# Optimization experiments

Measured on AMD Instinct MI355X. Metric: run time of the kernel, lower is better.

Reference implementation:

```python
import jax, jax.numpy as jnp
import numpy as np

B, N, DIM, H, D = 1, 1024, 512, 8, 64
BC, BS, K, W = 16, 16, 8, 256   # compress blk, selection blk, top-k blocks, sliding window
C = N // BC                     # number of compression / selection blocks
SCALE = D ** -0.5
EPS = 1e-6
NEG = -1e30


def rmsnorm(x):
    return x * jax.lax.rsqrt(jnp.mean(x * x, axis=-1, keepdims=True) + EPS)


def rope(x):  # x: [B,H,N,D], GPT-NeoX style half rotation
    half = D // 2
    inv = 1.0 / (10000.0 ** (jnp.arange(half, dtype=jnp.float32) / half))
    ang = jnp.arange(x.shape[2], dtype=jnp.float32)[:, None] * inv
    cos, sin = jnp.cos(ang), jnp.sin(ang)
    x1, x2 = x[..., :half], x[..., half:]
    return jnp.concatenate([x1 * cos - x2 * sin, x2 * cos + x1 * sin], axis=-1).astype(x.dtype)


def setup_inputs():
    key = jax.random.key(0)
    ks = jax.random.split(key, 24)
    w = lambda k, shape, fan: jax.random.normal(k, shape, jnp.float32) * (fan ** -0.5)
    return {
        'x':  jax.random.normal(ks[0], (B, N, DIM), jnp.float32),
        've': jax.random.normal(ks[1], (B, N, DIM), jnp.float32),
        'x0': jax.random.normal(ks[2], (B, N, DIM), jnp.float32),
        'lambdas': jnp.array([1.0, 0.0], jnp.float32),
        'Wq': w(ks[3], (DIM, H * D), DIM),
        'Wk': w(ks[4], (DIM, H * D), DIM),
        'Wv': w(ks[5], (DIM, H * D), DIM),
        'Wo': w(ks[6], (H * D, DIM), H * D),
        'Wg': w(ks[7], (DIM, 3 * H), DIM),
        'k_pos': w(ks[8], (H, BC, D), D),
        'v_pos': w(ks[9], (H, BC, D), D),
        'Wck': w(ks[10], (BC * D, D), BC * D),
        'bck': jnp.zeros((D,), jnp.float32),
        'Wcv': w(ks[11], (BC * D, D), BC * D),
        'bcv': jnp.zeros((D,), jnp.float32),
        'k_mem': w(ks[12], (H, 1, D), D),
        'v_mem': w(ks[13], (H, 1, D), D),
        'W1': w(ks[14], (DIM, 4 * DIM), DIM),
        'W2': w(ks[15], (4 * DIM, DIM), 4 * DIM),
    }


def _nsa_attn(xn, Wq, Wk, Wv, Wo, Wg, k_pos, v_pos, Wck, bck, Wcv, bcv, k_mem, v_mem):
    q = (xn @ Wq).reshape(B, N, H, D).transpose(0, 2, 1, 3)   # [B,H,N,D]
    k = (xn @ Wk).reshape(B, N, H, D).transpose(0, 2, 1, 3)
    v = (xn @ Wv).reshape(B, N, H, D).transpose(0, 2, 1, 3)
    q, k = rope(q), rope(k)
    i_idx = jnp.arange(N)

    # ---- compressed branch: pool kv into blocks via learned linear + intra-block pos emb ----
    kb = k.reshape(B, H, C, BC, D) + k_pos[None, :, None]
    vb = v.reshape(B, H, C, BC, D) + v_pos[None, :, None]
    ck = kb.reshape(B, H, C, BC * D) @ Wck + bck              # [B,H,C,D]
    cv = vb.reshape(B, H, C, BC * D) @ Wcv + bcv
    ckf = jnp.concatenate([jnp.broadcast_to(k_mem[None], (B, H, 1, D)), ck], axis=2)
    cvf = jnp.concatenate([jnp.broadcast_to(v_mem[None], (B, H, 1, D)), cv], axis=2)
    csim = jnp.einsum('bhid,bhjd->bhij', q, ckf) * SCALE      # [B,H,N,C+1]
    past = ((jnp.arange(C) + 1) * BC - 1)[None, :] < i_idx[:, None]   # block fully in the past
    cmask = jnp.concatenate([jnp.ones((N, 1), bool), past], axis=1)   # mem kv always visible
    cattn = jax.nn.softmax(jnp.where(cmask[None, None], csim, NEG), axis=-1)
    c_out = jnp.einsum('bhij,bhjd->bhid', cattn, cvf)

    # ---- fine selection branch: top-K blocks by compressed attention importance ----
    imp = jnp.where(past[None, None], cattn[..., 1:], NEG)    # [B,H,N,C]
    vals, sel = jax.lax.top_k(imp, K)                         # [B,H,N,K]
    valid = vals >= 0.0                                       # drop picks among masked blocks
    kb_f = k.reshape(B, H, C, BS, D)
    vb_f = v.reshape(B, H, C, BS, D)
    k_sel = jnp.take_along_axis(kb_f[:, :, None], sel[..., None, None], axis=3)  # [B,H,N,K,BS,D]
    v_sel = jnp.take_along_axis(vb_f[:, :, None], sel[..., None, None], axis=3)
    own = i_idx // BS                                         # query's own block, causal inside
    k_fine = jnp.concatenate([k_sel, kb_f[:, :, own][:, :, :, None]], axis=3)    # [B,H,N,K+1,BS,D]
    v_fine = jnp.concatenate([v_sel, vb_f[:, :, own][:, :, :, None]], axis=3)
    offs = jnp.arange(BS)
    m_sel = (sel[..., None] * BS + offs <= i_idx[None, None, :, None, None]) & valid[..., None]
    m_own = jnp.broadcast_to((own[:, None] * BS + offs <= i_idx[:, None])[None, None, :, None], (B, H, N, 1, BS))
    m_fine = jnp.concatenate([m_sel, m_own], axis=3)
    fsim = jnp.where(m_fine, jnp.einsum('bhnd,bhnksd->bhnks', q, k_fine) * SCALE, NEG)
    fattn = jax.nn.softmax(fsim.reshape(B, H, N, (K + 1) * BS), axis=-1).reshape(B, H, N, K + 1, BS)
    f_out = jnp.einsum('bhnks,bhnksd->bhnd', fattn, v_fine)

    # ---- sliding window branch ----
    smask = (i_idx[None, :] <= i_idx[:, None]) & (i_idx[:, None] - i_idx[None, :] < W)
    ssim = jnp.where(smask[None, None], jnp.einsum('bhid,bhjd->bhij', q, k) * SCALE, NEG)
    s_out = jnp.einsum('bhij,bhjd->bhid', jax.nn.softmax(ssim, axis=-1), v)

    # ---- per-head sigmoid gates combine the three strategies ----
    gates = jax.nn.sigmoid(xn @ Wg).reshape(B, N, H, 3).transpose(0, 2, 1, 3)  # [B,H,N,3]
    o = gates[..., 0:1] * c_out + gates[..., 1:2] * f_out + gates[..., 2:3] * s_out
    return o.transpose(0, 2, 1, 3).reshape(B, N, H * D) @ Wo


def reference(x, ve, x0, lambdas, Wq, Wk, Wv, Wo, Wg, k_pos, v_pos, Wck, bck, Wcv, bcv, k_mem, v_mem, W1, W2):
    # ve is accepted by NSABlock.forward but never consumed in this block
    x = lambdas[0] * x + lambdas[1] * x0
    x = x + _nsa_attn(rmsnorm(x), Wq, Wk, Wv, Wo, Wg, k_pos, v_pos, Wck, bck, Wcv, bcv, k_mem, v_mem)
    x = x + jnp.square(jax.nn.relu(rmsnorm(x) @ W1)) @ W2
    return x
```

## Files before the change

### kernel.cpp

```cpp
#include <hip/hip_runtime.h>
#include <math.h>

#define NTOK 1024
#define DIMM 512
#define NH 8
#define HD 64
#define BCB 16
#define BSB 16
#define KSEL 8
#define WWIN 256
#define CBLK 64
#define SCALE 0.125f
#define EPSV 1e-6f
#define NEGV -1e30f

typedef short bf16x8 __attribute__((ext_vector_type(8)));
typedef float f32x4 __attribute__((ext_vector_type(4)));

__device__ inline ushort f2b(float f) {
  union { float f; unsigned int u; } c; c.f = f;
  unsigned int u = c.u;
  return (ushort)((u + 0x7FFFu + ((u >> 16) & 1u)) >> 16);
}
__device__ inline float b2f(ushort h) {
// ... 201 lines not shown
  const int Kd = 2048;
  __shared__ ushort As[64 * 40];
  __shared__ ushort Bs[64 * 40];
  int tid = threadIdx.x;
  int lane = tid & 63, w = tid >> 6;
  int rb = blockIdx.y * 64, cb = blockIdx.x * 64;
  int kb = blockIdx.z * 1024;
  int wm = (w >> 1) * 32, wn = (w & 1) * 32;
  int quad = lane >> 4, l15 = lane & 15;
  int srow = tid >> 2, scol = (tid & 3) * 8;

  f32x4 acc[2][2];
#pragma unroll
  for (int i = 0; i < 2; i++)
#pragma unroll
    for (int j = 0; j < 2; j++) acc[i][j] = (f32x4){0.f, 0.f, 0.f, 0.f};

  const ushort* ap = A  + (size_t)(rb + srow) * Kd + kb + scol;
  const ushort* bp = BT + (size_t)(cb + srow) * Kd + kb + scol;
  ushort* aw = &As[srow * 40 + scol];
  ushort* bw = &Bs[srow * 40 + scol];

  int4 pa = *(const int4*)ap;
  int4 pb = *(const int4*)bp;

  for (int k0 = 0; k0 < 1024; k0 += 32) {
    if (k0) __syncthreads();
    *(int4*)aw = pa;
    *(int4*)bw = pb;
    __syncthreads();
    if (k0 + 32 < 1024) {
      pa = *(const int4*)(ap + k0 + 32);
      pb = *(const int4*)(bp + k0 + 32);
    }
    bf16x8 af[2], bfr[2];
#pragma unroll
    for (int t = 0; t < 2; t++) {
      af[t]  = *(const bf16x8*)&As[(wm + t * 16 + l15) * 40 + quad * 8];
      bfr[t] = *(const bf16x8*)&Bs[(wn + t * 16 + l15) * 40 + quad * 8];
    }
#pragma unroll
    for (int i = 0; i < 2; i++)
#pragma unroll
      for (int j = 0; j < 2; j++)
        acc[i][j] = __builtin_amdgcn_mfma_f32_16x16x32_bf16(af[i], bfr[j],
                                                            acc[i][j], 0, 0, 0);
  }

#pragma unroll
  for (int i = 0; i < 2; i++) {
#pragma unroll
    for (int j = 0; j < 2; j++) {
      int col = cb + wn + j * 16 + l15;
#pragma unroll
      for (int r = 0; r < 4; r++) {
        int row = rb + wm + i * 16 + quad * 4 + r;
        atomicAdd(&outb[(size_t)row * 512 + col], acc[i][j][r]);
      }
    }
  }
}

__global__ void __launch_bounds__(256)
k_gemm_wo(const float* __restrict__ cg, const float* __restrict__ fg,
          const float* __restrict__ sg, const float* __restrict__ gates,
          const ushort* __restrict__ BT, float* __restrict__ P0,
          float* __restrict__ P1) {
  __shared__ ushort As[64 * 40];
  __shared__ ushort Bs[64 * 40];
  int tid = threadIdx.x;
  int lane = tid & 63, wave = tid >> 6;
  int rb = blockIdx.y * 64, cb = blockIdx.x * 64;
  int kb = blockIdx.z * 256;
  int wm = (wave >> 1) * 32, wn = (wave & 1) * 32;
  int q = lane >> 4, l15 = lane & 15;
  int srow = tid >> 2, scol = (tid & 3) * 8;

  f32x4 acc[2][2];
#pragma unroll
  for (int i = 0; i < 2; i++)
#pragma unroll
    for (int j = 0; j < 2; j++) acc[i][j] = (f32x4){0.f, 0.f, 0.f, 0.f};

  int row = rb + srow;
  const ushort* bp = BT + (size_t)(cb + srow) * 512 + kb + scol;
  ushort* aw = &As[srow * 40 + scol];
  ushort* bw = &Bs[srow * 40 + scol];

  for (int k0 = 0; k0 < 256; k0 += 32) {
    int colb = kb + k0 + scol;
    int hh = colb >> 6;
    const float* gp = gates + (size_t)row * 24 + hh * 3;
    float g0 = gp[0], g1 = gp[1], g2 = gp[2];
    size_t off = (size_t)row * 512 + colb;
    float4 c0 = *(const float4*)(cg + off), c1 = *(const float4*)(cg + off + 4);
    float4 f0 = *(const float4*)(fg + off), f1 = *(const float4*)(fg + off + 4);
    float4 s0 = *(const float4*)(sg + off), s1 = *(const float4*)(sg + off + 4);
    float va[8] = {g0 * c0.x + g1 * f0.x + g2 * s0.x,
                   g0 * c0.y + g1 * f0.y + g2 * s0.y,
                   g0 * c0.z + g1 * f0.z + g2 * s0.z,
                   g0 * c0.w + g1 * f0.w + g2 * s0.w,
                   g0 * c1.x + g1 * f1.x + g2 * s1.x,
                   g0 * c1.y + g1 * f1.y + g2 * s1.y,
                   g0 * c1.z + g1 * f1.z + g2 * s1.z,
                   g0 * c1.w + g1 * f1.w + g2 * s1.w};
    ushort h[8];
#pragma unroll
    for (int e = 0; e < 8; e++) h[e] = f2b(va[e]);
    *(int4*)aw = *(int4*)h;
    *(int4*)bw = *(const int4*)(bp + k0);
    __syncthreads();
    bf16x8 af[2], bfr[2];
#pragma unroll
    for (int t = 0; t < 2; t++) {
      af[t]  = *(const bf16x8*)&As[(wm + t * 16 + l15) * 40 + q * 8];
      bfr[t] = *(const bf16x8*)&Bs[(wn + t * 16 + l15) * 40 + q * 8];
    }
#pragma unroll
    for (int i = 0; i < 2; i++)
#pragma unroll
      for (int j = 0; j < 2; j++)
        acc[i][j] = __builtin_amdgcn_mfma_f32_16x16x32_bf16(af[i], bfr[j],
                                                            acc[i][j], 0, 0, 0);
    __syncthreads();
  }

  float* pbuf = blockIdx.z ? P1 : P0;
#pragma unroll
  for (int i = 0; i < 2; i++) {
#pragma unroll
    for (int j = 0; j < 2; j++) {
      int col = cb + wn + j * 16 + l15;
#pragma unroll
      for (int r = 0; r < 4; r++) {
        int rr = rb + wm + i * 16 + q * 4 + r;
        pbuf[(size_t)rr * 512 + col] = acc[i][j][r];
      }
    }
  }
}

__global__ void __launch_bounds__(256)
k_gemm_qkv(const ushort* __restrict__ Ah, const ushort* __restrict__ Al,
           const ushort* __restrict__ BTh, const ushort* __restrict__ BTl,
           float* __restrict__ qout, ushort* __restrict__ khm_h,
           ushort* __restrict__ khm_l, ushort* __restrict__ vhm_h,
           ushort* __restrict__ vhm_l, float* __restrict__ gates,
           const float* __restrict__ ctab, const float* __restrict__ stab) {
  const int Kd = 512;
  __shared__ ushort SM[15360];
  ushort* Ash = SM;
  ushort* Asl = SM + 5120;
  ushort* Bsh = SM + 10240;
  ushort* Bsl = SM + 12800;
  int tid = threadIdx.x;
  int lane = tid & 63, wave = tid >> 6;
  int rb = blockIdx.y * 128, cb = blockIdx.x * 64;
  const bool prec = (cb < 1024);
  int wm = (wave >> 1) * 64, wn = (wave & 1) * 32;
  int q = lane >> 4, l15 = lane & 15;
  int srA = tid >> 1, scA = (tid & 1) * 16;
  int srB = tid >> 2, scB = (tid & 3) * 8;

  f32x4 acc[4][2];
#pragma unroll
  for (int i = 0; i < 4; i++)
#pragma unroll
    for (int j = 0; j < 2; j++) acc[i][j] = (f32x4){0.f, 0.f, 0.f, 0.f};

  const ushort* aph = Ah  + (size_t)(rb + srA) * Kd + scA;
  const ushort* apl = Al  + (size_t)(rb + srA) * Kd + scA;
  const ushort* bph = BTh + (size_t)(cb + srB) * Kd + scB;
  const ushort* bpl = BTl + (size_t)(cb + srB) * Kd + scB;
  ushort* awh = &Ash[srA * 40 + scA];
  ushort* awl = &Asl[srA * 40 + scA];
  ushort* bwh = &Bsh[srB * 40 + scB];
  ushort* bwl = &Bsl[srB * 40 + scB];

  int4 ph0 = *(const int4*)aph;
  int4 ph1 = *(const int4*)(aph + 8);
  int4 pbh = *(const int4*)bph;
  int4 pl0, pl1, pbl;
  if (prec) {
    pl0 = *(const int4*)apl;
    pl1 = *(const int4*)(apl + 8);
    pbl = *(const int4*)bpl;
  }

  for (int k0 = 0; k0 < Kd; k0 += 32) {
    if (k0) __syncthreads();
    *(int4*)awh = ph0; *(int4*)(awh + 8) = ph1;
    *(int4*)bwh = pbh;
    if (prec) {
      *(int4*)awl = pl0; *(int4*)(awl + 8) = pl1;
      *(int4*)bwl = pbl;
    }
    __syncthreads();
    if (k0 + 32 < Kd) {
      ph0 = *(const int4*)(aph + k0 + 32);
      ph1 = *(const int4*)(aph + k0 + 40);
      pbh = *(const int4*)(bph + k0 + 32);
      if (prec) {
        pl0 = *(const int4*)(apl + k0 + 32);
        pl1 = *(const int4*)(apl + k0 + 40);
        pbl = *(const int4*)(bpl + k0 + 32);
      }
    }
    bf16x8 afh[4], bfh[2], afl[4], bfl[2];
#pragma unroll
    for (int t = 0; t < 4; t++)
      afh[t] = *(const bf16x8*)&Ash[(wm + t * 16 + l15) * 40 + q * 8];
#pragma unroll
    for (int t = 0; t < 2; t++)
      bfh[t] = *(const bf16x8*)&Bsh[(wn + t * 16 + l15) * 40 + q * 8];
    if (prec) {
#pragma unroll
      for (int t = 0; t < 4; t++)
        afl[t] = *(const bf16x8*)&Asl[(wm + t * 16 + l15) * 40 + q * 8];
#pragma unroll
      for (int t = 0; t < 2; t++)
        bfl[t] = *(const bf16x8*)&Bsl[(wn + t * 16 + l15) * 40 + q * 8];
    }
#pragma unroll
    for (int i = 0; i < 4; i++)
#pragma unroll
      for (int j = 0; j < 2; j++) {
        acc[i][j] = __builtin_amdgcn_mfma_f32_16x16x32_bf16(afh[i], bfh[j],
                                                            acc[i][j], 0, 0, 0);
        if (prec) {
          acc[i][j] = __builtin_amdgcn_mfma_f32_16x16x32_bf16(afh[i], bfl[j],
                                                              acc[i][j], 0, 0, 0);
          acc[i][j] = __builtin_amdgcn_mfma_f32_16x16x32_bf16(afl[i], bfh[j],
                                                              acc[i][j], 0, 0, 0);
        }
      }
  }

  if (prec) {
    float* st = (float*)SM;
    int h = (cb & 511) >> 6;
#pragma unroll
    for (int hb = 0; hb < 2; hb++) {
      __syncthreads();
      if ((wave >> 1) == hb) {
#pragma unroll
        for (int i = 0; i < 4; i++)
#pragma unroll
          for (int j = 0; j < 2; j++)
#pragma unroll
            for (int r = 0; r < 4; r++)
              st[(i * 16 + q * 4 + r) * 66 + wn + j * 16 + l15] = acc[i][j][r];
      }
      __syncthreads();
#pragma unroll
      for (int e = 0; e < 8; e++) {
        int p = e * 256 + tid;
        int rw = p >> 5, d = p & 31;
        int n = rb + hb * 64 + rw;
        float x1 = st[rw * 66 + d], x2 = st[rw * 66 + d + 32];
        float cs = ctab[n * 32 + d], sn = stab[n * 32 + d];
        float o1 = x1 * cs - x2 * sn;
        float o2 = x2 * cs + x1 * sn;
        if (cb < 512) {
          qout[(size_t)n * 512 + h * 64 + d]      = o1;
          qout[(size_t)n * 512 + h * 64 + d + 32] = o2;
        } else {
          size_t ob = (size_t)h * 65536 + (size_t)n * 64 + d;
          ushort b1 = f2b(o1), b2v = f2b(o2);
          khm_h[ob]      = b1;
          khm_h[ob + 32] = b2v;
          khm_l[ob]      = f2b(o1 - b2f(b1));
          khm_l[ob + 32] = f2b(o2 - b2f(b2v));
        }
      }
    }
  } else {
#pragma unroll
    for (int i = 0; i < 4; i++) {
#pragma unroll
      for (int j = 0; j < 2; j++) {
        int col = cb + wn + j * 16 + l15;
#pragma unroll
        for (int r = 0; r < 4; r++) {
          int row = rb + wm + i * 16 + q * 4 + r;
          float vv = acc[i][j][r];
          if (cb >= 1536) {
            int c24 = col - 1536;
            if (c24 < 24)
              gates[(size_t)row * 24 + c24] = 1.f / (1.f + expf(-vv));
          } else {
            int c = col - 1024;
            size_t ob = (size_t)(c >> 6) * 65536 + (size_t)row * 64 + (c & 63);
            ushort hb = f2b(vv);
            vhm_h[ob] = hb;
            vhm_l[ob] = f2b(vv - b2f(hb));
          }
        }
      }
    }
  }
}

__global__ void __launch_bounds__(256)
k_mid(const ushort* __restrict__ khm_h, const ushort* __restrict__ khm_l,
      const ushort* __restrict__ vhm_h, const ushort* __restrict__ vhm_l,
      const ushort* __restrict__ WckTh, const ushort* __restrict__ WckTl,
      const ushort* __restrict__ WcvTh, const ushort* __restrict__ WcvTl,
      const float* __restrict__ pwk, const float* __restrict__ pwv,
      float* __restrict__ ckb, float* __restrict__ cvb,
      const float* __restrict__ qg, float* __restrict__ sout) {
  __shared__ union {
    struct { ushort Ash[32 * 72]; ushort Asl[32 * 72];
             ushort Bsh[64 * 72]; ushort Bsl[64 * 72]; } c;
    struct { ushort Kt[64 * 72]; ushort VT[64 * 72];
             ushort Qs[64 * 72]; ushort Ps[4][16 * 72]; } s;
  } U;
  int tid = threadIdx.x, lane = tid & 63, w = tid >> 6;
  int quad = lane >> 4, l15 = lane & 15;

  if (blockIdx.x < 32) {
    int h = blockIdx.x & 7, kv = (blockIdx.x >> 3) & 1, mh = blockIdx.x >> 4;
    const ushort* sH = kv ? vhm_h : khm_h;
    const ushort* sL = kv ? vhm_l : khm_l;
    const ushort* WTh = kv ? WcvTh : WckTh;
    const ushort* WTl = kv ? WcvTl : WckTl;
    const float* pw = (kv ? pwv : pwk) + h * 64;
    float* outp = kv ? cvb : ckb;

    ushort* Ash = U.c.Ash; ushort* Asl = U.c.Asl;
    ushort* Bsh = U.c.Bsh; ushort* Bsl = U.c.Bsl;
    int wmi = w >> 1, wnj = w & 1;
    int arow = tid >> 3, ae0 = (tid & 7) * 8;
    int brow = tid >> 2, be0 = (tid & 3) * 16;
    size_t abase = (size_t)h * 65536 + (size_t)(mh * 32 + arow) * 1024 + ae0;
    size_t bbase = (size_t)brow * 1024 + be0;

    f32x4 acc[2];
#pragma unroll
    for (int j = 0; j < 2; j++) acc[j] = (f32x4){0.f, 0.f, 0.f, 0.f};

    for (int t = 0; t < 16; t++) {
      int kb = t * 64;
      *(int4*)&Ash[arow * 72 + ae0] = *(const int4*)(sH + abase + kb);
      *(int4*)&Asl[arow * 72 + ae0] = *(const int4*)(sL + abase + kb);
      *(int4*)&Bsh[brow * 72 + be0]     = *(const int4*)(WTh + bbase + kb);
      *(int4*)&Bsh[brow * 72 + be0 + 8] = *(const int4*)(WTh + bbase + kb + 8);
      *(int4*)&Bsl[brow * 72 + be0]     = *(const int4*)(WTl + bbase + kb);
      *(int4*)&Bsl[brow * 72 + be0 + 8] = *(const int4*)(WTl + bbase + kb + 8);
      __syncthreads();
#pragma unroll
      for (int sub = 0; sub < 2; sub++) {
        int ar2 = (wmi * 16 + l15) * 72 + sub * 32 + quad * 8;
        bf16x8 afh = *(const bf16x8*)&Ash[ar2];
        bf16x8 afl = *(const bf16x8*)&Asl[ar2];
#pragma unroll
        for (int j = 0; j < 2; j++) {
          int br2 = (wnj * 32 + j * 16 + l15) * 72 + sub * 32 + quad * 8;
          bf16x8 bfh = *(const bf16x8*)&Bsh[br2];
          bf16x8 bfl = *(const bf16x8*)&Bsl[br2];
          acc[j] = __builtin_amdgcn_mfma_f32_16x16x32_bf16(afh, bfh, acc[j], 0, 0, 0);
          acc[j] = __builtin_amdgcn_mfma_f32_16x16x32_bf16(afh, bfl, acc[j], 0, 0, 0);
          acc[j] = __builtin_amdgcn_mfma_f32_16x16x32_bf16(afl, bfh, acc[j], 0, 0, 0);
        }
      }
      __syncthreads();
    }

#pragma unroll
    for (int j = 0; j < 2; j++) {
      int d = wnj * 32 + j * 16 + l15;
      float bv = pw[d];
#pragma unroll
      for (int r = 0; r < 4; r++) {
        int c = mh * 32 + wmi * 16 + quad * 4 + r;
        outp[((size_t)h * 64 + c) * 64 + d] = acc[j][r] + bv;
      }
    }
  } else {
    int sidx = blockIdx.x - 32;
    int h = sidx >> 4, i0 = (sidx & 15) * 64;
    ushort* Kt = U.s.Kt; ushort* VT = U.s.VT; ushort* Qs = U.s.Qs;

#pragma unroll
    for (int it = 0; it < 2; it++) {
      int f = it * 256 + tid;
      int r = f >> 3, d0 = (f & 7) * 8;
      const float* qp = qg + (size_t)(i0 + r) * DIMM + h * HD + d0;
      float4 t0 = *(const float4*)qp;
      float4 t1 = *(const float4*)(qp + 4);
      ushort u[8] = {f2b(t0.x), f2b(t0.y), f2b(t0.z), f2b(t0.w),
                     f2b(t1.x), f2b(t1.y), f2b(t1.z), f2b(t1.w)};
      *(int4*)&Qs[r * 72 + d0] = *(int4*)u;
    }

    int lo = i0 - (WWIN - 1); if (lo < 0) lo = 0;
    int jb_lo = lo >> 6, jb_hi = (i0 + 63) >> 6;

    float mrow[4], lrow[4];
    f32x4 Of[4];
#pragma unroll
    for (int r = 0; r < 4; r++) { mrow[r] = NEGV; lrow[r] = 0.f; }
#pragma unroll
    for (int d = 0; d < 4; d++) Of[d] = (f32x4){0.f, 0.f, 0.f, 0.f};

    for (int jb = jb_lo; jb <= jb_hi; jb++) {
      __syncthreads();
#pragma unroll
      for (int it = 0; it < 2; it++) {
        int f = it * 256 + tid;
        int r = f >> 3, c8 = (f & 7) * 8;
        const ushort* kp = khm_h + (size_t)h * 65536 + (size_t)(jb * 64 + r) * 64 + c8;
        *(int4*)&Kt[r * 72 + c8] = *(const int4*)kp;
        const ushort* vp = vhm_h + (size_t)h * 65536 + (size_t)(jb * 64 + r) * 64 + c8;
        ushort vv[8];
        *(int4*)vv = *(const int4*)vp;
#pragma unroll
        for (int e = 0; e < 8; e++) VT[(c8 + e) * 72 + r] = vv[e];
      }
      __syncthreads();

      bf16x8 qa[2];
#pragma unroll
      for (int c = 0; c < 2; c++)
        qa[c] = *(const bf16x8*)&Qs[(w * 16 + l15) * 72 + c * 32 + quad * 8];

      f32x4 sc[4];
      __builtin_amdgcn_s_setprio(1);
#pragma unroll
      for (int ks = 0; ks < 4; ks++) {
        f32x4 a = (f32x4){0.f, 0.f, 0.f, 0.f};
#pragma unroll
        for (int c = 0; c < 2; c++) {
          bf16x8 kb = *(const bf16x8*)&Kt[(ks * 16 + l15) * 72 + c * 32 + quad * 8];
          a = __builtin_amdgcn_mfma_f32_16x16x32_bf16(qa[c], kb, a, 0, 0, 0);
        }
        sc[ks] = a;
      }
      __builtin_amdgcn_s_setprio(0);

      float pm[4][4], rmax[4];
#pragma unroll
      for (int r = 0; r < 4; r++) rmax[r] = NEGV;
#pragma unroll
      for (int ks = 0; ks < 4; ks++) {
        int gj = jb * 64 + ks * 16 + l15;
#pragma unroll
        for (int r = 0; r < 4; r++) {
          int qi = i0 + w * 16 + quad * 4 + r;
          bool vis = (gj <= qi) && (qi - gj < WWIN);
          float s = vis ? sc[ks][r] * SCALE : NEGV;
          pm[ks][r] = s;
          rmax[r] = fmaxf(rmax[r], s);
        }
      }
#pragma unroll
      for (int off = 1; off < 16; off <<= 1)
#pragma unroll
        for (int r = 0; r < 4; r++)
          rmax[r] = fmaxf(rmax[r], __shfl_xor(rmax[r], off));

      float alpha[4], rsum[4];
#pragma unroll
      for (int r = 0; r < 4; r++) {
        float newm = fmaxf(mrow[r], rmax[r]);
        alpha[r] = expf(mrow[r] - newm);
        mrow[r] = newm;
        rsum[r] = 0.f;
      }
#pragma unroll
      for (int ks = 0; ks < 4; ks++)
#pragma unroll
        for (int r = 0; r < 4; r++) {
          float p = expf(pm[ks][r] - mrow[r]);
          pm[ks][r] = p;
          rsum[r] += p;
        }
#pragma unroll
      for (int off = 1; off < 16; off <<= 1)
#pragma unroll
        for (int r = 0; r < 4; r++)
          rsum[r] += __shfl_xor(rsum[r], off);
#pragma unroll
      for (int r = 0; r < 4; r++)
        lrow[r] = lrow[r] * alpha[r] + rsum[r];

#pragma unroll
      for (int ks = 0; ks < 4; ks++)
#pragma unroll
        for (int r = 0; r < 4; r++)
          U.s.Ps[w][(quad * 4 + r) * 72 + ks * 16 + l15] = f2b(pm[ks][r]);
#pragma unroll
      for (int d = 0; d < 4; d++)
#pragma unroll
        for (int r = 0; r < 4; r++)
          Of[d][r] *= alpha[r];

      __builtin_amdgcn_s_setprio(1);
#pragma unroll
      for (int c = 0; c < 2; c++) {
        bf16x8 pa = *(const bf16x8*)&U.s.Ps[w][l15 * 72 + c * 32 + quad * 8];
#pragma unroll
        for (int d = 0; d < 4; d++) {
          bf16x8 vb = *(const bf16x8*)&VT[(d * 16 + l15) * 72 + c * 32 + quad * 8];
          Of[d] = __builtin_amdgcn_mfma_f32_16x16x32_bf16(pa, vb, Of[d], 0, 0, 0);
        }
      }
      __builtin_amdgcn_s_setprio(0);
    }

#pragma unroll
    for (int d = 0; d < 4; d++)
#pragma unroll
      for (int r = 0; r < 4; r++) {
        int qi = i0 + w * 16 + quad * 4 + r;
        sout[(size_t)qi * DIMM + h * HD + d * 16 + l15] = Of[d][r] / lrow[r];
      }
  }
}

__global__ void __launch_bounds__(256)
k_cmpf(const float* __restrict__ qg, const float* __restrict__ ckb,
       const float* __restrict__ cvb, const float* __restrict__ k_mem,
       const float* __restrict__ v_mem, const ushort* __restrict__ khm_h,
       const ushort* __restrict__ vhm_h, float* __restrict__ cout,
       float* __restrict__ fout) {
  int h = blockIdx.y, i0 = blockIdx.x * 4;
  int tid = threadIdx.x, lane = tid & 63, w = tid >> 6;
  __shared__ float ckt[64][65];
  __shared__ float cvs[64][65];
  __shared__ float qs[4][64];
  __shared__ float kms[64], vms[64];
  __shared__ float sp[4][64];
  __shared__ float spf[4][144];

#pragma unroll
  for (int r = 0; r < 4; r++) {
    int f = r * 256 + tid;
    int c = f >> 4, d0 = (f & 15) * 4;
    float4 t = *(const float4*)(ckb + ((size_t)h * 64 + c) * 64 + d0);
    ckt[d0][c] = t.x; ckt[d0 + 1][c] = t.y; ckt[d0 + 2][c] = t.z; ckt[d0 + 3][c] = t.w;
    float4 u = *(const float4*)(cvb + ((size_t)h * 64 + c) * 64 + d0);
    cvs[c][d0] = u.x; cvs[c][d0 + 1] = u.y; cvs[c][d0 + 2] = u.z; cvs[c][d0 + 3] = u.w;
  }
  if (tid < 64) {
    int r = tid >> 4, d0 = (tid & 15) * 4;
    float4 t = *(const float4*)(qg + (size_t)(i0 + r) * DIMM + h * HD + d0);
    qs[r][d0] = t.x; qs[r][d0 + 1] = t.y; qs[r][d0 + 2] = t.z; qs[r][d0 + 3] = t.w;
  } else if (tid < 128) {
    kms[tid - 64] = k_mem[h * HD + tid - 64];
  } else if (tid < 192) {
    vms[tid - 128] = v_mem[h * HD + tid - 128];
  }
  __syncthreads();

  const ushort* kbase = khm_h + (size_t)h * 65536;
  const ushort* vbase = vhm_h + (size_t)h * 65536;

  int qi = i0 + w;
  {
    float dot = 0.f, dm = 0.f;
#pragma unroll 8
    for (int e = 0; e < 64; e++) {
      float qe = qs[w][e];
      dot = fmaf(qe, ckt[e][lane], dot);
      dm  = fmaf(qe, kms[e], dm);
    }
    bool vis = (lane * BCB + BCB - 1) < qi;
    float sj = vis ? dot * SCALE : NEGV;
    float smem = dm * SCALE;
    float m = wred_max(fmaxf(sj, smem));
    float p = expf(sj - m);
    float pmem = expf(smem - m);
    float l = wred_sum(p) + pmem;
    float inv = 1.f / l;

    int selreg = -1;
    float impv = vis ? p : NEGV;
#pragma unroll
    for (int kk = 0; kk < KSEL; kk++) {
      float bv = impv; int bi = lane;
#pragma unroll
      for (int off = 32; off > 0; off >>= 1) {
        float ov = __shfl_xor(bv, off);
        int   oi = __shfl_xor(bi, off);
        if (ov > bv || (ov == bv && oi < bi)) { bv = ov; bi = oi; }
      }
      if (lane == kk) selreg = (bv >= 0.f) ? bi : -1;
      if (lane == bi) impv = NEGV;
    }

    sp[w][lane] = p;
    float od = pmem * vms[lane];
#pragma unroll 8
    for (int j = 0; j < 64; j++) od = fmaf(sp[w][j], cvs[j][lane], od);
    cout[(size_t)qi * DIMM + h * HD + lane] = od * inv;

    int own = qi >> 4;
    float slv[3];
#pragma unroll
    for (int t = 0; t < 3; t++) {
      int key = t * 64 + lane;
      float sv = NEGV;
      if (key < 144) {
        int kk = key >> 4, krow = key & 15;
        int bidx; bool fvis;
        if (kk < KSEL) {
          bidx = __shfl(selreg, kk);
          fvis = (bidx >= 0);
          if (!fvis) bidx = 0;
        } else {
          bidx = own;
          fvis = (krow <= (qi & 15));
        }
        const ushort* kr = kbase + (size_t)(bidx * BSB + krow) * 64;
        float fd = 0.f;
#pragma unroll
        for (int e8 = 0; e8 < 8; e8++) {
          ushort kv8[8];
          *(int4*)kv8 = *(const int4*)(kr + e8 * 8);
#pragma unroll
          for (int e = 0; e < 8; e++)
            fd = fmaf(qs[w][e8 * 8 + e], b2f(kv8[e]), fd);
        }
        sv = fvis ? fd * SCALE : NEGV;
      }
      slv[t] = sv;
    }
    float fm = wred_max(fmaxf(fmaxf(slv[0], slv[1]), slv[2]));
    float fsum = 0.f;
#pragma unroll
    for (int t = 0; t < 3; t++) {
      int key = t * 64 + lane;
      if (key < 144) {
        float pv = expf(slv[t] - fm);
        spf[w][key] = pv;
        fsum += pv;
      }
    }
    fsum = wred_sum(fsum);
    float finv = 1.f / fsum;

    float facc = 0.f;
#pragma unroll
    for (int kk = 0; kk < KSEL + 1; kk++) {
      int bidx = (kk < KSEL) ? __shfl(selreg, kk) : own;
      if (bidx < 0) bidx = 0;
      const ushort* vr = vbase + (size_t)(bidx * BSB) * 64 + lane;
#pragma unroll 8
      for (int krow = 0; krow < 16; krow++)
        facc = fmaf(spf[w][kk * 16 + krow], b2f(vr[(size_t)krow * 64]), facc);
    }
    fout[(size_t)qi * DIMM + h * HD + lane] = facc * finv;
  }
}

extern "C" void kernel_launch(void* const* d_in, const int* in_sizes, int n_in,
                              void* d_out, int out_size, void* d_ws, size_t ws_size,
                              hipStream_t stream) {
  const float* x     = (const float*)d_in[0];
  const float* ve    = (const float*)d_in[1]; (void)ve;
  const float* x0    = (const float*)d_in[2];
  const float* lam   = (const float*)d_in[3];
  const float* Wq    = (const float*)d_in[4];
  const float* Wk    = (const float*)d_in[5];
  const float* Wv    = (const float*)d_in[6];
  const float* Wo    = (const float*)d_in[7];
  const float* Wg    = (const float*)d_in[8];
  const float* k_pos = (const float*)d_in[9];
  const float* v_pos = (const float*)d_in[10];
  const float* Wck   = (const float*)d_in[11];
  const float* bck   = (const float*)d_in[12];
  const float* Wcv   = (const float*)d_in[13];
  const float* bcv   = (const float*)d_in[14];
  const float* k_mem = (const float*)d_in[15];
  const float* v_mem = (const float*)d_in[16];
  const float* W1    = (const float*)d_in[17];
  const float* W2    = (const float*)d_in[18];
  float* out = (float*)d_out;
  float* ws  = (float*)d_ws;

  const size_t NW = (size_t)NTOK * DIMM;
  float* xr    = ws;
  float* xn    = ws + 1 * NW;
  float* q     = ws + 2 * NW;
  float* kslot = ws + 3 * NW;
  float* vslot = ws + 4 * NW;
  float* coutb = ws + 5 * NW;
  float* foutb = ws + 6 * NW;
  float* soutb = ws + 7 * NW;
  float* gates = ws + 9 * NW;
  float* ckb   = gates + 32768;
  float* cvb   = ckb + 32768;
  ushort* qkvTh = (ushort*)(cvb + 32768 + 65536);
  ushort* qkvTl = qkvTh + 1600 * 512;
  ushort* WoT   = qkvTl + 1600 * 512;
  ushort* W1T   = WoT   + 512 * 512;
  ushort* W2T   = W1T   + 2048 * 512;
  ushort* WckTh = W2T   + 512 * 2048;
  ushort* WckTl = WckTh + 64 * 1024;
  ushort* WcvTh = WckTl + 64 * 1024;
  ushort* WcvTl = WcvTh + 64 * 1024;
  float* ctab   = (float*)(WcvTl + 64 * 1024);
  float* stab   = ctab + 32768;
  float* pwk    = stab + 32768;
  float* pwv    = pwk + 512;

  ushort* xnh = (ushort*)xn;
  ushort* xnl = xnh + NW;
  ushort* khm_h = (ushort*)kslot;
  ushort* khm_l = khm_h + 524288;
  ushort* vhm_h = (ushort*)vslot;
  ushort* vhm_l = vhm_h + 524288;
  float* p0w = kslot;
  float* p1w = q;
  ushort* ybf = (ushort*)soutb;
  ushort* h1b = (ushort*)q;

  WtrPack pk;
  pk.d[0] = {Wq, qkvTh,              qkvTl,              512, 512,  512};
  pk.d[1] = {Wk, qkvTh + 512 * 512,  qkvTl + 512 * 512,  512, 512,  512};
  pk.d[2] = {Wv, qkvTh + 1024 * 512, qkvTl + 1024 * 512, 512, 512,  512};
  pk.d[3] = {Wo, WoT, nullptr,  512, 512,  512};
  pk.d[4] = {W1, W1T, nullptr,  512, 2048, 2048};
  pk.d[5] = {W2, W2T, nullptr, 2048, 512,  512};
  pk.d[6] = {Wck, WckTh, WckTl, 1024, 64, 64};
  pk.d[7] = {Wcv, WcvTh, WcvTl, 1024, 64, 64};
  pk.d[8] = {Wg, qkvTh + 1536 * 512, qkvTl + 1536 * 512, 512, 24, 64};
  int cum = 0;
  for (int e = 0; e < 9; e++) {
    cum += (pk.d[e].Npad / 32) * (pk.d[e].K / 32);
    pk.cum[e] = cum;
  }

  k_pre<<<cum + NTOK + 128 + 16, 256, 0, stream>>>(
      pk, x, x0, lam, xr, xnh, xnl, ctab, stab,
      k_pos, v_pos, Wck, Wcv, bck, bcv, pwk, pwv);

  k_gemm_qkv<<<dim3(25, NTOK / 128), 256, 0, stream>>>(
      xnh, xnl, qkvTh, qkvTl, q, khm_h, khm_l, vhm_h, vhm_l, gates,
      ctab, stab);

  k_mid<<<160, 256, 0, stream>>>(khm_h, khm_l, vhm_h, vhm_l,
                                 WckTh, WckTl, WcvTh, WcvTl,
                                 pwk, pwv, ckb, cvb, q, soutb);

  k_cmpf<<<dim3(NTOK / 4, NH), 256, 0, stream>>>(
      q, ckb, cvb, k_mem, v_mem, khm_h, vhm_h, coutb, foutb);

  k_gemm_wo<<<dim3(512 / 64, NTOK / 64, 2), 256, 0, stream>>>(
      coutb, foutb, soutb, gates, WoT, p0w, p1w);
  k_rms_bf<<<NTOK, 256, 0, stream>>>(xr, p0w, p1w, out, ybf);

  k_gemm_w1<<<dim3(2048 / 64, NTOK / 128), 256, 0, stream>>>(ybf, W1T, h1b);
  k_gemm_w2<<<dim3(512 / 64, NTOK / 64, 2), 256, 0, stream>>>(h1b, W2T, out);
}
```

Before: 240.6 us.

## Regroup mid-stage kernels: split ckcv GEMM, co-launch sliding-window with compressed/fine attention

The former k_mid kernel fused the compression GEMM (32 blocks) with the sliding-window attention (128 blocks), and k_cmpf ran afterwards. Now the compression GEMM runs alone in a small kernel, and the sliding-window attention is merged with the compressed/fine attention into one 2176-block launch that shares a shared-memory union. The intent is to overlap the sliding-window work with the compressed/selected branch, which depends on the GEMM output, rather than with the short GEMM. The trade-off is a 32-block launch that leaves most of the GPU idle, and a larger shared-memory union that may lower occupancy for the many small compressed-branch blocks.

```diff
diff --git a/kernel.cpp b/kernel.cpp
--- a/kernel.cpp
+++ b/kernel.cpp
@@ -527,82 +527,91 @@
 }
 
 __global__ void __launch_bounds__(256)
-k_mid(const ushort* __restrict__ khm_h, const ushort* __restrict__ khm_l,
-      const ushort* __restrict__ vhm_h, const ushort* __restrict__ vhm_l,
-      const ushort* __restrict__ WckTh, const ushort* __restrict__ WckTl,
-      const ushort* __restrict__ WcvTh, const ushort* __restrict__ WcvTl,
-      const float* __restrict__ pwk, const float* __restrict__ pwv,
-      float* __restrict__ ckb, float* __restrict__ cvb,
-      const float* __restrict__ qg, float* __restrict__ sout) {
+k_ckcv(const ushort* __restrict__ khm_h, const ushort* __restrict__ khm_l,
+       const ushort* __restrict__ vhm_h, const ushort* __restrict__ vhm_l,
+       const ushort* __restrict__ WckTh, const ushort* __restrict__ WckTl,
+       const ushort* __restrict__ WcvTh, const ushort* __restrict__ WcvTl,
+       const float* __restrict__ pwk, const float* __restrict__ pwv,
+       float* __restrict__ ckb, float* __restrict__ cvb) {
+  __shared__ ushort Ash[32 * 72], Asl[32 * 72];
+  __shared__ ushort Bsh[64 * 72], Bsl[64 * 72];
+  int tid = threadIdx.x, lane = tid & 63, w = tid >> 6;
+  int quad = lane >> 4, l15 = lane & 15;
+  int h = blockIdx.x & 7, kv = (blockIdx.x >> 3) & 1, mh = blockIdx.x >> 4;
+  const ushort* sH = kv ? vhm_h : khm_h;
+  const ushort* sL = kv ? vhm_l : khm_l;
+  const ushort* WTh = kv ? WcvTh : WckTh;
+  const ushort* WTl = kv ? WcvTl : WckTl;
+  const float* pw = (kv ? pwv : pwk) + h * 64;
+  float* outp = kv ? cvb : ckb;
+
+  int wmi = w >> 1, wnj = w & 1;
+  int arow = tid >> 3, ae0 = (tid & 7) * 8;
+  int brow = tid >> 2, be0 = (tid & 3) * 16;
+  size_t abase = (size_t)h * 65536 + (size_t)(mh * 32 + arow) * 1024 + ae0;
+  size_t bbase = (size_t)brow * 1024 + be0;
+
+  f32x4 acc[2];
+#pragma unroll
+  for (int j = 0; j < 2; j++) acc[j] = (f32x4){0.f, 0.f, 0.f, 0.f};
+
+  for (int t = 0; t < 16; t++) {
+    int kb = t * 64;
+    *(int4*)&Ash[arow * 72 + ae0] = *(const int4*)(sH + abase + kb);
+    *(int4*)&Asl[arow * 72 + ae0] = *(const int4*)(sL + abase + kb);
+    *(int4*)&Bsh[brow * 72 + be0]     = *(const int4*)(WTh + bbase + kb);
+    *(int4*)&Bsh[brow * 72 + be0 + 8] = *(const int4*)(WTh + bbase + kb + 8);
+    *(int4*)&Bsl[brow * 72 + be0]     = *(const int4*)(WTl + bbase + kb);
+    *(int4*)&Bsl[brow * 72 + be0 + 8] = *(const int4*)(WTl + bbase + kb + 8);
+    __syncthreads();
+#pragma unroll
+    for (int sub = 0; sub < 2; sub++) {
+      int ar2 = (wmi * 16 + l15) * 72 + sub * 32 + quad * 8;
+      bf16x8 afh = *(const bf16x8*)&Ash[ar2];
+      bf16x8 afl = *(const bf16x8*)&Asl[ar2];
+#pragma unroll
+      for (int j = 0; j < 2; j++) {
+        int br2 = (wnj * 32 + j * 16 + l15) * 72 + sub * 32 + quad * 8;
+        bf16x8 bfh = *(const bf16x8*)&Bsh[br2];
+        bf16x8 bfl = *(const bf16x8*)&Bsl[br2];
+        acc[j] = __builtin_amdgcn_mfma_f32_16x16x32_bf16(afh, bfh, acc[j], 0, 0, 0);
+        acc[j] = __builtin_amdgcn_mfma_f32_16x16x32_bf16(afh, bfl, acc[j], 0, 0, 0);
+        acc[j] = __builtin_amdgcn_mfma_f32_16x16x32_bf16(afl, bfh, acc[j], 0, 0, 0);
+      }
+    }
+    __syncthreads();
+  }
+
+#pragma unroll
+  for (int j = 0; j < 2; j++) {
+    int d = wnj * 32 + j * 16 + l15;
+    float bv = pw[d];
+#pragma unroll
+    for (int r = 0; r < 4; r++) {
+      int c = mh * 32 + wmi * 16 + quad * 4 + r;
+      outp[((size_t)h * 64 + c) * 64 + d] = acc[j][r] + bv;
+    }
+  }
+}
+
+__global__ void __launch_bounds__(256)
+k_scf(const float* __restrict__ qg, const ushort* __restrict__ khm_h,
+      const ushort* __restrict__ vhm_h, float* __restrict__ sout,
+      const float* __restrict__ ckb, const float* __restrict__ cvb,
+      const float* __restrict__ k_mem, const float* __restrict__ v_mem,
+      float* __restrict__ cout, float* __restrict__ fout) {
   __shared__ union {
-    struct { ushort Ash[32 * 72]; ushort Asl[32 * 72];
-             ushort Bsh[64 * 72]; ushort Bsl[64 * 72]; } c;
     struct { ushort Kt[64 * 72]; ushort VT[64 * 72];
              ushort Qs[64 * 72]; ushort Ps[4][16 * 72]; } s;
+    struct { float ckt[64][65]; float cvs[64][65]; float qs[4][64];
+             float kms[64]; float vms[64]; float sp[4][64];
+             float spf[4][144]; } c;
   } U;
   int tid = threadIdx.x, lane = tid & 63, w = tid >> 6;
   int quad = lane >> 4, l15 = lane & 15;
 
-  if (blockIdx.x < 32) {
-    int h = blockIdx.x & 7, kv = (blockIdx.x >> 3) & 1, mh = blockIdx.x >> 4;
-    const ushort* sH = kv ? vhm_h : khm_h;
-    const ushort* sL = kv ? vhm_l : khm_l;
-    const ushort* WTh = kv ? WcvTh : WckTh;
-    const ushort* WTl = kv ? WcvTl : WckTl;
-    const float* pw = (kv ? pwv : pwk) + h * 64;
-    float* outp = kv ? cvb : ckb;
-
-    ushort* Ash = U.c.Ash; ushort* Asl = U.c.Asl;
-    ushort* Bsh = U.c.Bsh; ushort* Bsl = U.c.Bsl;
-    int wmi = w >> 1, wnj = w & 1;
-    int arow = tid >> 3, ae0 = (tid & 7) * 8;
-    int brow = tid >> 2, be0 = (tid & 3) * 16;
-    size_t abase = (size_t)h * 65536 + (size_t)(mh * 32 + arow) * 1024 + ae0;
-    size_t bbase = (size_t)brow * 1024 + be0;
-
-    f32x4 acc[2];
-#pragma unroll
-    for (int j = 0; j < 2; j++) acc[j] = (f32x4){0.f, 0.f, 0.f, 0.f};
-
-    for (int t = 0; t < 16; t++) {
-      int kb = t * 64;
-      *(int4*)&Ash[arow * 72 + ae0] = *(const int4*)(sH + abase + kb);
-      *(int4*)&Asl[arow * 72 + ae0] = *(const int4*)(sL + abase + kb);
-      *(int4*)&Bsh[brow * 72 + be0]     = *(const int4*)(WTh + bbase + kb);
-      *(int4*)&Bsh[brow * 72 + be0 + 8] = *(const int4*)(WTh + bbase + kb + 8);
-      *(int4*)&Bsl[brow * 72 + be0]     = *(const int4*)(WTl + bbase + kb);
-      *(int4*)&Bsl[brow * 72 + be0 + 8] = *(const int4*)(WTl + bbase + kb + 8);
-      __syncthreads();
-#pragma unroll
-      for (int sub = 0; sub < 2; sub++) {
-        int ar2 = (wmi * 16 + l15) * 72 + sub * 32 + quad * 8;
-        bf16x8 afh = *(const bf16x8*)&Ash[ar2];
-        bf16x8 afl = *(const bf16x8*)&Asl[ar2];
-#pragma unroll
-        for (int j = 0; j < 2; j++) {
-          int br2 = (wnj * 32 + j * 16 + l15) * 72 + sub * 32 + quad * 8;
-          bf16x8 bfh = *(const bf16x8*)&Bsh[br2];
-          bf16x8 bfl = *(const bf16x8*)&Bsl[br2];
-          acc[j] = __builtin_amdgcn_mfma_f32_16x16x32_bf16(afh, bfh, acc[j], 0, 0, 0);
-          acc[j] = __builtin_amdgcn_mfma_f32_16x16x32_bf16(afh, bfl, acc[j], 0, 0, 0);
-          acc[j] = __builtin_amdgcn_mfma_f32_16x16x32_bf16(afl, bfh, acc[j], 0, 0, 0);
-        }
-      }
-      __syncthreads();
-    }
-
-#pragma unroll
-    for (int j = 0; j < 2; j++) {
-      int d = wnj * 32 + j * 16 + l15;
-      float bv = pw[d];
-#pragma unroll
-      for (int r = 0; r < 4; r++) {
-        int c = mh * 32 + wmi * 16 + quad * 4 + r;
-        outp[((size_t)h * 64 + c) * 64 + d] = acc[j][r] + bv;
-      }
-    }
-  } else {
-    int sidx = blockIdx.x - 32;
+  if (blockIdx.x < 128) {
+    int sidx = blockIdx.x;
     int h = sidx >> 4, i0 = (sidx & 15) * 64;
     ushort* Kt = U.s.Kt; ushort* VT = U.s.VT; ushort* Qs = U.s.Qs;
 
@@ -726,7 +735,7 @@
         bf16x8 pa = *(const bf16x8*)&U.s.Ps[w][l15 * 72 + c * 32 + quad * 8];
 #pragma unroll
         for (int d = 0; d < 4; d++) {
-          bf16x8 vb = *(const bf16x8*)&VT[(d * 16 + l15) * 72 + c * 32 + quad * 8];
+          bf16x8 vb = *(const bf16x8*)&U.s.VT[(d * 16 + l15) * 72 + c * 32 + quad * 8];
           Of[d] = __builtin_amdgcn_mfma_f32_16x16x32_bf16(pa, vb, Of[d], 0, 0, 0);
         }
       }
@@ -740,142 +749,132 @@
         int qi = i0 + w * 16 + quad * 4 + r;
         sout[(size_t)qi * DIMM + h * HD + d * 16 + l15] = Of[d][r] / lrow[r];
       }
-  }
-}
-
-__global__ void __launch_bounds__(256)
-k_cmpf(const float* __restrict__ qg, const float* __restrict__ ckb,
-       const float* __restrict__ cvb, const float* __restrict__ k_mem,
-       const float* __restrict__ v_mem, const ushort* __restrict__ khm_h,
-       const ushort* __restrict__ vhm_h, float* __restrict__ cout,
-       float* __restrict__ fout) {
-  int h = blockIdx.y, i0 = blockIdx.x * 4;
-  int tid = threadIdx.x, lane = tid & 63, w = tid >> 6;
-  __shared__ float ckt[64][65];
-  __shared__ float cvs[64][65];
-  __shared__ float qs[4][64];
-  __shared__ float kms[64], vms[64];
-  __shared__ float sp[4][64];
-  __shared__ float spf[4][144];
-
-#pragma unroll
-  for (int r = 0; r < 4; r++) {
-    int f = r * 256 + tid;
-    int c = f >> 4, d0 = (f & 15) * 4;
-    float4 t = *(const float4*)(ckb + ((size_t)h * 64 + c) * 64 + d0);
-    ckt[d0][c] = t.x; ckt[d0 + 1][c] = t.y; ckt[d0 + 2][c] = t.z; ckt[d0 + 3][c] = t.w;
-    float4 u = *(const float4*)(cvb + ((size_t)h * 64 + c) * 64 + d0);
-    cvs[c][d0] = u.x; cvs[c][d0 + 1] = u.y; cvs[c][d0 + 2] = u.z; cvs[c][d0 + 3] = u.w;
-  }
-  if (tid < 64) {
-    int r = tid >> 4, d0 = (tid & 15) * 4;
-    float4 t = *(const float4*)(qg + (size_t)(i0 + r) * DIMM + h * HD + d0);
-    qs[r][d0] = t.x; qs[r][d0 + 1] = t.y; qs[r][d0 + 2] = t.z; qs[r][d0 + 3] = t.w;
-  } else if (tid < 128) {
-    kms[tid - 64] = k_mem[h * HD + tid - 64];
-  } else if (tid < 192) {
-    vms[tid - 128] = v_mem[h * HD + tid - 128];
-  }
-  __syncthreads();
-
-  const ushort* kbase = khm_h + (size_t)h * 65536;
-  const ushort* vbase = vhm_h + (size_t)h * 65536;
-
-  int qi = i0 + w;
-  {
-    float dot = 0.f, dm = 0.f;
+  } else {
+    int idx = blockIdx.x - 128;
+    int h = idx >> 8, i0 = (idx & 255) * 4;
+
+#pragma unroll
+    for (int r = 0; r < 4; r++) {
+      int f = r * 256 + tid;
+      int c = f >> 4, d0 = (f & 15) * 4;
+      float4 t = *(const float4*)(ckb + ((size_t)h * 64 + c) * 64 + d0);
+      U.c.ckt[d0][c] = t.x; U.c.ckt[d0 + 1][c] = t.y;
+      U.c.ckt[d0 + 2][c] = t.z; U.c.ckt[d0 + 3][c] = t.w;
+      float4 u = *(const float4*)(cvb + ((size_t)h * 64 + c) * 64 + d0);
+      U.c.cvs[c][d0] = u.x; U.c.cvs[c][d0 + 1] = u.y;
+      U.c.cvs[c][d0 + 2] = u.z; U.c.cvs[c][d0 + 3] = u.w;
+    }
+    if (tid < 64) {
+      int r = tid >> 4, d0 = (tid & 15) * 4;
+      float4 t = *(const float4*)(qg + (size_t)(i0 + r) * DIMM + h * HD + d0);
+      U.c.qs[r][d0] = t.x; U.c.qs[r][d0 + 1] = t.y;
+      U.c.qs[r][d0 + 2] = t.z; U.c.qs[r][d0 + 3] = t.w;
+    } else if (tid < 128) {
+      U.c.kms[tid - 64] = k_mem[h * HD + tid - 64];
+    } else if (tid < 192) {
+      U.c.vms[tid - 128] = v_mem[h * HD + tid - 128];
+    }
+    __syncthreads();
+
+    const ushort* kbase = khm_h + (size_t)h * 65536;
+    const ushort* vbase = vhm_h + (size_t)h * 65536;
+
+    int qi = i0 + w;
+    {
+      float dot = 0.f, dm = 0.f;
 #pragma unroll 8
-    for (int e = 0; e < 64; e++) {
-      float qe = qs[w][e];
-      dot = fmaf(qe, ckt[e][lane], dot);
-      dm  = fmaf(qe, kms[e], dm);
-    }
-    bool vis = (lane * BCB + BCB - 1) < qi;
-    float sj = vis ? dot * SCALE : NEGV;
-    float smem = dm * SCALE;
-    float m = wred_max(fmaxf(sj, smem));
-    float p = expf(sj - m);
-    float pmem = expf(smem - m);
-    float l = wred_sum(p) + pmem;
-    float inv = 1.f / l;
-
-    int selreg = -1;
-    float impv = vis ? p : NEGV;
-#pragma unroll
-    for (int kk = 0; kk < KSEL; kk++) {
-      float bv = impv; int bi = lane;
-#pragma unroll
-      for (int off = 32; off > 0; off >>= 1) {
-        float ov = __shfl_xor(bv, off);
-        int   oi = __shfl_xor(bi, off);
-        if (ov > bv || (ov == bv && oi < bi)) { bv = ov; bi = oi; }
-      }
-      if (lane == kk) selreg = (bv >= 0.f) ? bi : -1;
-      if (lane == bi) impv = NEGV;
-    }
-
-    sp[w][lane] = p;
-    float od = pmem * vms[lane];
+      for (int e = 0; e < 64; e++) {
+        float qe = U.c.qs[w][e];
+        dot = fmaf(qe, U.c.ckt[e][lane], dot);
+        dm  = fmaf(qe, U.c.kms[e], dm);
+      }
+      bool vis = (lane * BCB + BCB - 1) < qi;
+      float sj = vis ? dot * SCALE : NEGV;
+      float smem = dm * SCALE;
+      float m = wred_max(fmaxf(sj, smem));
+      float p = expf(sj - m);
+      float pmem = expf(smem - m);
+      float l = wred_sum(p) + pmem;
+      float inv = 1.f / l;
+
+      int selreg = -1;
+      float impv = vis ? p : NEGV;
+#pragma unroll
+      for (int kk = 0; kk < KSEL; kk++) {
+        float bv = impv; int bi = lane;
+#pragma unroll
+        for (int off = 32; off > 0; off >>= 1) {
+          float ov = __shfl_xor(bv, off);
+          int   oi = __shfl_xor(bi, off);
+          if (ov > bv || (ov == bv && oi < bi)) { bv = ov; bi = oi; }
+        }
+        if (lane == kk) selreg = (bv >= 0.f) ? bi : -1;
+        if (lane == bi) impv = NEGV;
+      }
+
+      U.c.sp[w][lane] = p;
+      float od = pmem * U.c.vms[lane];
 #pragma unroll 8
-    for (int j = 0; j < 64; j++) od = fmaf(sp[w][j], cvs[j][lane], od);
-    cout[(size_t)qi * DIMM + h * HD + lane] = od * inv;
-
-    int own = qi >> 4;
-    float slv[3];
-#pragma unroll
-    for (int t = 0; t < 3; t++) {
-      int key = t * 64 + lane;
-      float sv = NEGV;
-      if (key < 144) {
-        int kk = key >> 4, krow = key & 15;
-        int bidx; bool fvis;
-        if (kk < KSEL) {
-          bidx = __shfl(selreg, kk);
-          fvis = (bidx >= 0);
-          if (!fvis) bidx = 0;
-        } else {
-          bidx = own;
-          fvis = (krow <= (qi & 15));
+      for (int j = 0; j < 64; j++) od = fmaf(U.c.sp[w][j], U.c.cvs[j][lane], od);
+      cout[(size_t)qi * DIMM + h * HD + lane] = od * inv;
+
+      int own = qi >> 4;
+      float slv[3];
+#pragma unroll
+      for (int t = 0; t < 3; t++) {
+        int key = t * 64 + lane;
+        float sv = NEGV;
+        if (key < 144) {
+          int kk = key >> 4, krow = key & 15;
+          int bidx; bool fvis;
+          if (kk < KSEL) {
+            bidx = __shfl(selreg, kk);
+            fvis = (bidx >= 0);
+            if (!fvis) bidx = 0;
+          } else {
+            bidx = own;
+            fvis = (krow <= (qi & 15));
+          }
+          const ushort* kr = kbase + (size_t)(bidx * BSB + krow) * 64;
+          float fd = 0.f;
+#pragma unroll
+          for (int e8 = 0; e8 < 8; e8++) {
+            ushort kv8[8];
+            *(int4*)kv8 = *(const int4*)(kr + e8 * 8);
+#pragma unroll
+            for (int e = 0; e < 8; e++)
+              fd = fmaf(U.c.qs[w][e8 * 8 + e], b2f(kv8[e]), fd);
+          }
+          sv = fvis ? fd * SCALE : NEGV;
         }
-        const ushort* kr = kbase + (size_t)(bidx * BSB + krow) * 64;
-        float fd = 0.f;
-#pragma unroll
-        for (int e8 = 0; e8 < 8; e8++) {
-          ushort kv8[8];
-          *(int4*)kv8 = *(const int4*)(kr + e8 * 8);
-#pragma unroll
-          for (int e = 0; e < 8; e++)
-            fd = fmaf(qs[w][e8 * 8 + e], b2f(kv8[e]), fd);
+        slv[t] = sv;
+      }
+      float fm = wred_max(fmaxf(fmaxf(slv[0], slv[1]), slv[2]));
+      float fsum = 0.f;
+#pragma unroll
+      for (int t = 0; t < 3; t++) {
+        int key = t * 64 + lane;
+        if (key < 144) {
+          float pv = expf(slv[t] - fm);
+          U.c.spf[w][key] = pv;
+          fsum += pv;
         }
-        sv = fvis ? fd * SCALE : NEGV;
-      }
-      slv[t] = sv;
-    }
-    float fm = wred_max(fmaxf(fmaxf(slv[0], slv[1]), slv[2]));
-    float fsum = 0.f;
-#pragma unroll
-    for (int t = 0; t < 3; t++) {
-      int key = t * 64 + lane;
-      if (key < 144) {
-        float pv = expf(slv[t] - fm);
-        spf[w][key] = pv;
-        fsum += pv;
-      }
-    }
-    fsum = wred_sum(fsum);
-    float finv = 1.f / fsum;
-
-    float facc = 0.f;
-#pragma unroll
-    for (int kk = 0; kk < KSEL + 1; kk++) {
-      int bidx = (kk < KSEL) ? __shfl(selreg, kk) : own;
-      if (bidx < 0) bidx = 0;
-      const ushort* vr = vbase + (size_t)(bidx * BSB) * 64 + lane;
+      }
+      fsum = wred_sum(fsum);
+      float finv = 1.f / fsum;
+
+      float facc = 0.f;
+#pragma unroll
+      for (int kk = 0; kk < KSEL + 1; kk++) {
+        int bidx = (kk < KSEL) ? __shfl(selreg, kk) : own;
+        if (bidx < 0) bidx = 0;
+        const ushort* vr = vbase + (size_t)(bidx * BSB) * 64 + lane;
 #pragma unroll 8
-      for (int krow = 0; krow < 16; krow++)
-        facc = fmaf(spf[w][kk * 16 + krow], b2f(vr[(size_t)krow * 64]), facc);
-    }
-    fout[(size_t)qi * DIMM + h * HD + lane] = facc * finv;
+        for (int krow = 0; krow < 16; krow++)
+          facc = fmaf(U.c.spf[w][kk * 16 + krow], b2f(vr[(size_t)krow * 64]), facc);
+      }
+      fout[(size_t)qi * DIMM + h * HD + lane] = facc * finv;
+    }
   }
 }
 
@@ -965,12 +964,12 @@
       xnh, xnl, qkvTh, qkvTl, q, khm_h, khm_l, vhm_h, vhm_l, gates,
       ctab, stab);
 
-  k_mid<<<160, 256, 0, stream>>>(khm_h, khm_l, vhm_h, vhm_l,
+  k_ckcv<<<32, 256, 0, stream>>>(khm_h, khm_l, vhm_h, vhm_l,
                                  WckTh, WckTl, WcvTh, WcvTl,
-                                 pwk, pwv, ckb, cvb, q, soutb);
-
-  k_cmpf<<<dim3(NTOK / 4, NH), 256, 0, stream>>>(
-      q, ckb, cvb, k_mem, v_mem, khm_h, vhm_h, coutb, foutb);
+                                 pwk, pwv, ckb, cvb);
+
+  k_scf<<<128 + 2048, 256, 0, stream>>>(q, khm_h, vhm_h, soutb,
+                                        ckb, cvb, k_mem, v_mem, coutb, foutb);
 
   k_gemm_wo<<<dim3(512 / 64, NTOK / 64, 2), 256, 0, stream>>>(
       coutb, foutb, soutb, gates, WoT, p0w, p1w);
```

Result: slower. 265.5 us (+10.4%).
